# Kernel optimization log

Measured on AMD Instinct MI355X. Metric: run time of the kernel, lower is better.

The kernel has to match this reference:

```python
import jax, jax.numpy as jnp
import numpy as np

CODEBOOK_DIM = 8192
EMBED_DIM = 256
TEMP = 1.0
KL_WEIGHT = 5e-4
EPS = 1e-10


def setup_inputs() -> dict:
    key = jax.random.key(0)
    k1, k2, k3 = jax.random.split(key, 3)
    b, n, h, w = 8, CODEBOOK_DIM, 32, 32
    z = jax.random.normal(k1, (b, n, h, w), dtype=jnp.float32)
    # torch init: uniform(-1/codebook_dim, 1/codebook_dim)
    embed_weight = jax.random.uniform(
        k2, (n, EMBED_DIM), dtype=jnp.float32,
        minval=-1.0 / CODEBOOK_DIM, maxval=1.0 / CODEBOOK_DIM)
    gumbel_noise = jax.random.gumbel(k3, (b, n, h, w), dtype=jnp.float32)
    return {"z": z, "embed_weight": embed_weight, "gumbel_noise": gumbel_noise}


def reference(z, embed_weight, gumbel_noise):
    n = z.shape[1]
    # F.gumbel_softmax(z, tau, dim=1, hard=True): soft + straight-through hard one-hot
    logits = (z + gumbel_noise) / TEMP
    soft = jax.nn.softmax(logits, axis=1)          # (b, n, h, w)
    ind = jnp.argmax(logits, axis=1)               # (b, h, w) == argmax of soft
    hard = jax.nn.one_hot(ind, n, axis=1, dtype=z.dtype)
    y = hard - jax.lax.stop_gradient(soft) + soft  # straight-through estimator
    # codebook contraction: 'b n h w, n d -> b d h w'
    z_q = jnp.einsum('bnhw,nd->bdhw', y, embed_weight)
    # KL(qy || uniform) * kl_weight
    qy = jax.nn.softmax(z, axis=1)
    diff = KL_WEIGHT * jnp.mean(jnp.sum(qy * jnp.log(qy * n + EPS), axis=1))
    return z_q, diff, ind
```

## Files before the change

kernel.cpp:

```cpp
#include <hip/hip_runtime.h>
#include <math.h>

#define N_CH   8192
#define N_PIX  8192
#define SCH    32
#define OUT_ZQ   0
#define OUT_DIFF 2097152
#define OUT_IND  2097153
#define LOG_N 9.010913348f

__global__ __launch_bounds__(256) void k1_partial(
    const float* __restrict__ z, const float* __restrict__ gn,
    float* __restrict__ wsM, int* __restrict__ wsI,
    float* __restrict__ wsZ, float* __restrict__ wsS)
{
    const int tile = blockIdx.x;
    const int sch  = blockIdx.y;
    const int t    = threadIdx.x;
    const int grp  = t & 63;
    const int sub  = t >> 6;

    const int p0 = tile * 256 + grp * 4;
    const int b  = p0 >> 10;
    const int q0 = p0 & 1023;
    const int n0 = sch * 256 + sub * 64;
    const float* zp = z  + (size_t)b * (N_CH * 1024) + q0;
    const float* gp = gn + (size_t)b * (N_CH * 1024) + q0;

    float m0 = -INFINITY, m1 = -INFINITY, m2 = -INFINITY, m3 = -INFINITY;
    int   i0 = 0, i1 = 0, i2 = 0, i3 = 0;
    float za = 0.f, zb = 0.f, zc = 0.f, zd = 0.f;
    float sa = 0.f, sb = 0.f, sc = 0.f, sd = 0.f;

    #pragma unroll 4
    for (int j = 0; j < 64; ++j) {
        const int n = n0 + j;
        const float4 zv = *(const float4*)(zp + (size_t)n * 1024);
        const float4 gv = *(const float4*)(gp + (size_t)n * 1024);
        float l, e;
        l = zv.x + gv.x; if (l > m0) { m0 = l; i0 = n; }
        e = __expf(zv.x); za += e; sa = fmaf(e, zv.x, sa);
        l = zv.y + gv.y; if (l > m1) { m1 = l; i1 = n; }
        e = __expf(zv.y); zb += e; sb = fmaf(e, zv.y, sb);
        l = zv.z + gv.z; if (l > m2) { m2 = l; i2 = n; }
        e = __expf(zv.z); zc += e; sc = fmaf(e, zv.z, sc);
        l = zv.w + gv.w; if (l > m3) { m3 = l; i3 = n; }
        e = __expf(zv.w); zd += e; sd = fmaf(e, zv.w, sd);
    }

    __shared__ float lm[4][256];
    __shared__ int   li[4][256];
    __shared__ float lz[4][256];
    __shared__ float ls[4][256];
    const int pl = grp * 4;
    lm[sub][pl+0] = m0; lm[sub][pl+1] = m1; lm[sub][pl+2] = m2; lm[sub][pl+3] = m3;
    li[sub][pl+0] = i0; li[sub][pl+1] = i1; li[sub][pl+2] = i2; li[sub][pl+3] = i3;
    lz[sub][pl+0] = za; lz[sub][pl+1] = zb; lz[sub][pl+2] = zc; lz[sub][pl+3] = zd;
    ls[sub][pl+0] = sa; ls[sub][pl+1] = sb; ls[sub][pl+2] = sc; ls[sub][pl+3] = sd;
    __syncthreads();

    float M = -INFINITY; int I = 0; float Z = 0.f, S = 0.f;
    #pragma unroll
    for (int s = 0; s < 4; ++s) {
        const float mm = lm[s][t];
        if (mm > M) { M = mm; I = li[s][t]; }
        Z += lz[s][t];
        S += ls[s][t];
    }
    const int p = tile * 256 + t;
    wsM[sch * N_PIX + p] = M;
    wsI[sch * N_PIX + p] = I;
    wsZ[sch * N_PIX + p] = Z;
    wsS[sch * N_PIX + p] = S;
}

__global__ __launch_bounds__(256) void k2_final(
    const float* __restrict__ wsM, const int* __restrict__ wsI,
    const float* __restrict__ wsZ, const float* __restrict__ wsS,
    float* __restrict__ out, int* __restrict__ wsInd, float* __restrict__ wsKl)
{
    const int p = blockIdx.x * 256 + threadIdx.x;
    float M = -INFINITY; int I = 0; float Z = 0.f, S = 0.f;
    for (int s = 0; s < SCH; ++s) {
        const float mm = wsM[s * N_PIX + p];
        const int   ii = wsI[s * N_PIX + p];
        if (mm > M) { M = mm; I = ii; }
        Z += wsZ[s * N_PIX + p];
        S += wsS[s * N_PIX + p];
    }
    out[OUT_IND + p] = (float)I;
    wsInd[p] = I;
    const float kl = S / Z - __logf(Z) + LOG_N;

    __shared__ float red[256];
    red[threadIdx.x] = kl;
    __syncthreads();
    for (int off = 128; off > 0; off >>= 1) {
        if (threadIdx.x < off) red[threadIdx.x] += red[threadIdx.x + off];
        __syncthreads();
    }
    if (threadIdx.x == 0) wsKl[blockIdx.x] = red[0];
}

__global__ void k3_diff(const float* __restrict__ wsKl, float* __restrict__ out)
{
    float v = (threadIdx.x < 32) ? wsKl[threadIdx.x] : 0.f;
    #pragma unroll
    for (int off = 32; off > 0; off >>= 1) v += __shfl_down(v, off);
    if (threadIdx.x == 0) out[OUT_DIFF] = 5e-4f * (v * (1.0f / 8192.0f));
}

__global__ __launch_bounds__(256) void k4_zq(
    const float* __restrict__ emb, const int* __restrict__ indi,
    float* __restrict__ out)
{
    const int b = blockIdx.x >> 5;
    const int h = blockIdx.x & 31;
    const int t = threadIdx.x;

    __shared__ int   rows[32];
    __shared__ float tile[32 * 257];
    if (t < 32) rows[t] = indi[b * 1024 + h * 32 + t];
    __syncthreads();

    for (int j = 0; j < 32; ++j) {
        const int r = rows[j];
        tile[j * 257 + t] = emb[r * 256 + t];
    }
    __syncthreads();

    const int w  = t & 31;
    const int dg = t >> 5;
    const int obase = b * (256 * 1024) + h * 32 + w;
    #pragma unroll 4
    for (int k = 0; k < 32; ++k) {
        const int d = dg + k * 8;
        out[obase + d * 1024] = tile[w * 257 + d];
    }
}

extern "C" void kernel_launch(void* const* d_in, const int* in_sizes, int n_in,
                              void* d_out, int out_size, void* d_ws, size_t ws_size,
                              hipStream_t stream)
{
    const float* z   = (const float*)d_in[0];
    const float* emb = (const float*)d_in[1];
    const float* gn  = (const float*)d_in[2];
    float* out = (float*)d_out;

    char* ws = (char*)d_ws;
    float* wsM   = (float*)(ws);
    int*   wsI   = (int*)  (ws + (1u << 20));
    float* wsZ   = (float*)(ws + (2u << 20));
    float* wsS   = (float*)(ws + (3u << 20));
    int*   wsInd = (int*)  (ws + (4u << 20));
    float* wsKl  = (float*)(ws + (4u << 20) + 65536);

    k1_partial<<<dim3(32, 32), 256, 0, stream>>>(z, gn, wsM, wsI, wsZ, wsS);
    k2_final  <<<32, 256, 0, stream>>>(wsM, wsI, wsZ, wsS, out, wsInd, wsKl);
    k3_diff   <<<1, 64, 0, stream>>>(wsKl, out);
    k4_zq     <<<256, 256, 0, stream>>>(emb, wsInd, out);
}
```

Measured before the change: 549.0 us.

## Double channel splits, batch loads in k1, fold diff reduction into zq kernel

The channel dimension is now split into 64 chunks instead of 32, doubling the k1 grid to 2048 blocks so more loads are in flight across the GPU. Each thread issues four float4 loads of z and noise up front before computing, to increase memory-level parallelism. The one-block KL reduction kernel is merged into the z_q gather kernel as an extra block, removing one launch. The trade-off is twice the workspace partials written by k1 and read by k2, plus more registers per thread.

```diff
diff --git a/kernel.cpp b/kernel.cpp
--- a/kernel.cpp
+++ b/kernel.cpp
@@ -3,7 +3,7 @@
 
 #define N_CH   8192
 #define N_PIX  8192
-#define SCH    32
+#define SCH    64
 #define OUT_ZQ   0
 #define OUT_DIFF 2097152
 #define OUT_IND  2097153
@@ -23,29 +23,35 @@
     const int p0 = tile * 256 + grp * 4;
     const int b  = p0 >> 10;
     const int q0 = p0 & 1023;
-    const int n0 = sch * 256 + sub * 64;
-    const float* zp = z  + (size_t)b * (N_CH * 1024) + q0;
-    const float* gp = gn + (size_t)b * (N_CH * 1024) + q0;
+    const int n0 = sch * 128 + sub * 32;
+    const float* zp = z  + (size_t)b * (N_CH * 1024) + (size_t)n0 * 1024 + q0;
+    const float* gp = gn + (size_t)b * (N_CH * 1024) + (size_t)n0 * 1024 + q0;
 
     float m0 = -INFINITY, m1 = -INFINITY, m2 = -INFINITY, m3 = -INFINITY;
     int   i0 = 0, i1 = 0, i2 = 0, i3 = 0;
-    float za = 0.f, zb = 0.f, zc = 0.f, zd = 0.f;
-    float sa = 0.f, sb = 0.f, sc = 0.f, sd = 0.f;
+    float za = 0.f, zsb = 0.f, zc = 0.f, zd = 0.f;
+    float sa = 0.f, ssb = 0.f, sc = 0.f, sd = 0.f;
 
-    #pragma unroll 4
-    for (int j = 0; j < 64; ++j) {
-        const int n = n0 + j;
-        const float4 zv = *(const float4*)(zp + (size_t)n * 1024);
-        const float4 gv = *(const float4*)(gp + (size_t)n * 1024);
-        float l, e;
-        l = zv.x + gv.x; if (l > m0) { m0 = l; i0 = n; }
-        e = __expf(zv.x); za += e; sa = fmaf(e, zv.x, sa);
-        l = zv.y + gv.y; if (l > m1) { m1 = l; i1 = n; }
-        e = __expf(zv.y); zb += e; sb = fmaf(e, zv.y, sb);
-        l = zv.z + gv.z; if (l > m2) { m2 = l; i2 = n; }
-        e = __expf(zv.z); zc += e; sc = fmaf(e, zv.z, sc);
-        l = zv.w + gv.w; if (l > m3) { m3 = l; i3 = n; }
-        e = __expf(zv.w); zd += e; sd = fmaf(e, zv.w, sd);
+    for (int j = 0; j < 32; j += 4) {
+        float4 zv[4], gv[4];
+        #pragma unroll
+        for (int u = 0; u < 4; ++u) {
+            zv[u] = *(const float4*)(zp + (size_t)(j + u) * 1024);
+            gv[u] = *(const float4*)(gp + (size_t)(j + u) * 1024);
+        }
+        #pragma unroll
+        for (int u = 0; u < 4; ++u) {
+            const int n = n0 + j + u;
+            float l, e;
+            l = zv[u].x + gv[u].x; if (l > m0) { m0 = l; i0 = n; }
+            e = __expf(zv[u].x); za  += e; sa  = fmaf(e, zv[u].x, sa);
+            l = zv[u].y + gv[u].y; if (l > m1) { m1 = l; i1 = n; }
+            e = __expf(zv[u].y); zsb += e; ssb = fmaf(e, zv[u].y, ssb);
+            l = zv[u].z + gv[u].z; if (l > m2) { m2 = l; i2 = n; }
+            e = __expf(zv[u].z); zc  += e; sc  = fmaf(e, zv[u].z, sc);
+            l = zv[u].w + gv[u].w; if (l > m3) { m3 = l; i3 = n; }
+            e = __expf(zv[u].w); zd  += e; sd  = fmaf(e, zv[u].w, sd);
+        }
     }
 
     __shared__ float lm[4][256];
@@ -55,8 +61,8 @@
     const int pl = grp * 4;
     lm[sub][pl+0] = m0; lm[sub][pl+1] = m1; lm[sub][pl+2] = m2; lm[sub][pl+3] = m3;
     li[sub][pl+0] = i0; li[sub][pl+1] = i1; li[sub][pl+2] = i2; li[sub][pl+3] = i3;
-    lz[sub][pl+0] = za; lz[sub][pl+1] = zb; lz[sub][pl+2] = zc; lz[sub][pl+3] = zd;
-    ls[sub][pl+0] = sa; ls[sub][pl+1] = sb; ls[sub][pl+2] = sc; ls[sub][pl+3] = sd;
+    lz[sub][pl+0] = za; lz[sub][pl+1] = zsb; lz[sub][pl+2] = zc; lz[sub][pl+3] = zd;
+    ls[sub][pl+0] = sa; ls[sub][pl+1] = ssb; ls[sub][pl+2] = sc; ls[sub][pl+3] = sd;
     __syncthreads();
 
     float M = -INFINITY; int I = 0; float Z = 0.f, S = 0.f;
@@ -102,18 +108,20 @@
     if (threadIdx.x == 0) wsKl[blockIdx.x] = red[0];
 }
 
-__global__ void k3_diff(const float* __restrict__ wsKl, float* __restrict__ out)
-{
-    float v = (threadIdx.x < 32) ? wsKl[threadIdx.x] : 0.f;
-    #pragma unroll
-    for (int off = 32; off > 0; off >>= 1) v += __shfl_down(v, off);
-    if (threadIdx.x == 0) out[OUT_DIFF] = 5e-4f * (v * (1.0f / 8192.0f));
-}
-
 __global__ __launch_bounds__(256) void k4_zq(
     const float* __restrict__ emb, const int* __restrict__ indi,
-    float* __restrict__ out)
+    const float* __restrict__ wsKl, float* __restrict__ out)
 {
+    if (blockIdx.x == 256) {
+        if (threadIdx.x < 64) {
+            float v = (threadIdx.x < 32) ? wsKl[threadIdx.x] : 0.f;
+            #pragma unroll
+            for (int off = 32; off > 0; off >>= 1) v += __shfl_down(v, off);
+            if (threadIdx.x == 0) out[OUT_DIFF] = 5e-4f * (v * (1.0f / 8192.0f));
+        }
+        return;
+    }
+
     const int b = blockIdx.x >> 5;
     const int h = blockIdx.x & 31;
     const int t = threadIdx.x;
@@ -150,14 +158,13 @@
 
     char* ws = (char*)d_ws;
     float* wsM   = (float*)(ws);
-    int*   wsI   = (int*)  (ws + (1u << 20));
-    float* wsZ   = (float*)(ws + (2u << 20));
-    float* wsS   = (float*)(ws + (3u << 20));
-    int*   wsInd = (int*)  (ws + (4u << 20));
-    float* wsKl  = (float*)(ws + (4u << 20) + 65536);
+    int*   wsI   = (int*)  (ws + (2u << 20));
+    float* wsZ   = (float*)(ws + (4u << 20));
+    float* wsS   = (float*)(ws + (6u << 20));
+    int*   wsInd = (int*)  (ws + (8u << 20));
+    float* wsKl  = (float*)(ws + (8u << 20) + 65536);
 
-    k1_partial<<<dim3(32, 32), 256, 0, stream>>>(z, gn, wsM, wsI, wsZ, wsS);
+    k1_partial<<<dim3(32, SCH), 256, 0, stream>>>(z, gn, wsM, wsI, wsZ, wsS);
     k2_final  <<<32, 256, 0, stream>>>(wsM, wsI, wsZ, wsS, out, wsInd, wsKl);
-    k3_diff   <<<1, 64, 0, stream>>>(wsKl, out);
-    k4_zq     <<<256, 256, 0, stream>>>(emb, wsInd, out);
+    k4_zq     <<<257, 256, 0, stream>>>(emb, wsInd, wsKl, out);
 }
```

New measurement: 557.1 us. About the same (+1.5%).
